# Performance work log

Measured on AMD Instinct MI355X. Metric: run time of the kernel, lower is better.

The kernel has to match this reference:

```python
import jax, jax.numpy as jnp
import numpy as np

# Config matching init_kwargs: input_shape=(C,T,H,W)=(512,32,14,14), window_size=9, n_heads=8
B, C, T, H, W = 2, 512, 32, 14, 14
N, K = 8, 9
CI = C // N              # per-head inter channels (64)
P = (K - 1) // 2         # symmetric temporal zero-pad so S == T


def setup_inputs() -> dict:
    key = jax.random.key(0)
    ks = jax.random.split(key, 7)
    s = 0.02
    return {
        "x":  jax.random.normal(ks[0], (B, C, T, H, W), jnp.float32),
        # per-head 1x1x1 conv (Linear3d) weights/biases, stacked over heads
        "Wq": jax.random.normal(ks[1], (N, CI, C), jnp.float32) * s,
        "bq": jax.random.normal(ks[2], (N, CI), jnp.float32) * s,
        "Wk": jax.random.normal(ks[3], (N, CI, C), jnp.float32) * s,
        "bk": jax.random.normal(ks[4], (N, CI), jnp.float32) * s,
        "Wv": jax.random.normal(ks[5], (N, CI, C), jnp.float32) * s,
        "bv": jax.random.normal(ks[6], (N, CI), jnp.float32) * s,
    }


def reference(x, Wq, bq, Wk, bk, Wv, bv):
    # x: (B, C, T, H, W). Dropout (p=0.25) is inference-mode identity.
    Bx, Cx, Tx, Hx, Wd = x.shape
    HW = Hx * Wd
    xf = x.reshape(Bx, Cx, Tx, HW)

    # Queries: every original frame is the center of its own window -> project x directly.
    q = jnp.einsum('bctp,nic->bnitp', xf, Wq) + bq[None, :, :, None, None]  # (B,N,ci,T,HW)

    # Keys/values on temporally zero-padded input (Pad3d gives S == T windows).
    xp = jnp.pad(xf, ((0, 0), (0, 0), (P, P), (0, 0)))  # (B,C,T+K-1,HW)
    k = jnp.einsum('bctp,nic->bnitp', xp, Wk) + bk[None, :, :, None, None]
    v = jnp.einsum('bctp,nic->bnitp', xp, Wv) + bv[None, :, :, None, None]

    # Sliding windows over padded time: window s covers padded frames s..s+K-1
    win = jnp.arange(Tx)[:, None] + jnp.arange(K)[None, :]  # (T,K)
    kw = k[:, :, :, win]  # (B,N,ci,T,K,HW)
    vw = v[:, :, :, win].reshape(Bx, N, CI, Tx, K * HW)

    # alpha[b,n,t,p,m] = sum_i q[b,n,i,t,p] * k_win[b,n,i,t,m]; softmax over keys m
    alpha = jnp.einsum('bnitp,bnitkm->bntpkm', q, kw).reshape(Bx, N, Tx, HW, K * HW)
    alpha = jax.nn.softmax(alpha, axis=-1)

    # y = alpha @ value -> (B,N,ci,T,HW); head concat is channel-major reshape
    y = jnp.einsum('bntpm,bnitm->bnitp', alpha, vw)
    z = y.reshape(Bx, Cx, Tx, Hx, Wd) + x  # residual
    return z
```

## Files before the change

kernel.cpp:

```cpp
#include <hip/hip_runtime.h>
#include <hip/hip_bf16.h>
#include <stdint.h>
#include <cstddef>

#define BB  2
#define CC  512
#define TT  32
#define HWP 196
#define NH  8
#define KWIN 9
#define CID 64
#define PPAD 4
#define TP  40
#define MTOT 12544
#define NTOT 1536
#define VSLOT 224
#define LOG2E 1.44269504f

typedef unsigned short u16;
typedef unsigned int   u32;
typedef __attribute__((ext_vector_type(8))) short short8;
typedef __attribute__((ext_vector_type(4))) float floatx4;

__device__ __forceinline__ u16 f2bf(float f) {
    u32 u = __float_as_uint(f);
    u32 r = (u + 0x7fffu + ((u >> 16) & 1u)) >> 16;
    return (u16)r;
}
__device__ __forceinline__ u32 pack2bf(float a, float b) {
    return (u32)f2bf(a) | ((u32)f2bf(b) << 16);
}
__device__ __forceinline__ u32 packtrunc(float a, float b) {
    return __builtin_amdgcn_perm(__float_as_uint(b), __float_as_uint(a), 0x07060302u);
}
__device__ __forceinline__ float fexp2(float x) {
    return __builtin_amdgcn_exp2f(x);
}
__device__ __forceinline__ void gload16(const u16* g, u16* l) {
    __builtin_amdgcn_global_load_lds(
        (const __attribute__((address_space(1))) u32*)g,
        (__attribute__((address_space(3))) u32*)l, 16, 0, 0);
}

__global__ __launch_bounds__(256) void prep_transpose(
    const float* __restrict__ x, u16* __restrict__ xt,
    const float* __restrict__ Wq, const float* __restrict__ Wk,
    const float* __restrict__ Wv, u16* __restrict__ Wbf,
    const float* __restrict__ bk, const float* __restrict__ bv,
    u16* __restrict__ Kout, u16* __restrict__ Vtp)
{
    __shared__ float T[64 * 197];
    int bxg = blockIdx.x;
    int tid = threadIdx.x;

    if (bxg < BB * TT * 8) {
        int bx = bxg;
        int ct = bx & 7; bx >>= 3;
        int t = bx & 31;
        int b = bx >> 5;
        const float* src = x + ((size_t)(b * CC + ct * 64) * TT + t) * HWP;
        for (int i = tid; i < 64 * 49; i += 256) {
            int c = i / 49;
            int p4 = i - c * 49;
            float4 v = *(const float4*)(src + (size_t)c * (TT * HWP) + p4 * 4);
            float* Tp = &T[c * 197 + p4 * 4];
            Tp[0] = v.x; Tp[1] = v.y; Tp[2] = v.z; Tp[3] = v.w;
        }
        __syncthreads();
        u16* dst = xt + (size_t)((b * TT + t) * HWP) * CC + ct * 64;
        for (int i = tid; i < HWP * 8; i += 256) {
            int p = i >> 3;
            int c0 = (i & 7) * 8;
            u32 w[4];
            #pragma unroll
            for (int k = 0; k < 4; k++)
                w[k] = pack2bf(T[(c0 + 2 * k) * 197 + p],
                               T[(c0 + 2 * k + 1) * 197 + p]);
            *(uint4*)(dst + (size_t)p * CC + c0) = *(uint4*)w;
        }
        return;
    }

    int id = (bxg - BB * TT * 8) * 256 + tid;
    const int wtot = NTOT * CC / 2;
    const int kper = 2 * NH * 8 * HWP * 32;
    const int vper = 2 * NH * 8 * 64 * (VSLOT/2);
    if (id < wtot) {
        int c2 = id & 255;
        int oc = id >> 8;
        int kind = oc >> 9;
        int idx = oc & 511;
        const float* src = (kind == 0 ? Wq : (kind == 1 ? Wk : Wv)) + (size_t)idx * CC + c2 * 2;
        ((u32*)Wbf)[id] = pack2bf(src[0], src[1]);
    } else if (id < wtot + kper) {
        int i = id - wtot;
        int ci2 = i & 31; i >>= 5;
        int p = i % HWP;  i /= HWP;
        int fr = i & 7;   i >>= 3;
        int head = i & 7;
        int b = i >> 3;
        int tp = fr < 4 ? fr : fr + 32;
        const float* bias = bk + head * CID + ci2 * 2;
        size_t addr = (((size_t)(b * NH + head) * TP + tp) * HWP + p) * 32 + ci2;
        ((u32*)Kout)[addr] = pack2bf(bias[0], bias[1]);
    } else if (id < wtot + kper + vper) {
        int i = id - wtot - kper;
        int s2 = i % (VSLOT/2); i /= (VSLOT/2);
        int ci = i & 63; i >>= 6;
        int fr = i & 7;  i >>= 3;
        int head = i & 7;
        int b = i >> 3;
        int tp = fr < 4 ? fr : fr + 32;
        float bias = bv[head * CID + ci];
        size_t addr = (((size_t)(b * NH + head) * TP + tp) * 64 + ci) * (VSLOT/2) + s2;
        ((u32*)Vtp)[addr] = pack2bf(bias, bias);
    }
}

__global__ __launch_bounds__(512) void proj_gemm2(
    const u16* __restrict__ xt, const u16* __restrict__ Wbf,
    const float* __restrict__ bq, const float* __restrict__ bk,
    const float* __restrict__ bv,
    u16* __restrict__ Qout, u16* __restrict__ Kout, u16* __restrict__ Vtp)
{
    __shared__ u16 sA[128 * 64];
    __shared__ u16 sB[256 * 64];

    int bx = blockIdx.x;
    int nb = bx % 6;
    int mt = bx / 6;
    int tid = threadIdx.x;
    int wave = tid >> 6, lane = tid & 63, quad = lane >> 4, l15 = lane & 15;
    int wm = wave >> 2, wn = wave & 3;
    int mbase = mt * 128 + wm * 64;
    int nbase = nb * 256 + wn * 64;

    int lr = lane >> 3;
    int sw = ((lane & 7) * 8) ^ (lr << 3);

    floatx4 acc[4][4];
    #pragma unroll
    for (int ms = 0; ms < 4; ms++)
        #pragma unroll
        for (int ns = 0; ns < 4; ns++)
            acc[ms][ns] = (floatx4){0.f, 0.f, 0.f, 0.f};

    const u16* abase = xt + (size_t)(mt * 128) * CC;
    const u16* bbase = Wbf + (size_t)(nb * 256) * CC;

    for (int kc = 0; kc < 8; kc++) {
        __syncthreads();
        #pragma unroll
        for (int i = 0; i < 2; i++) {
            int rbase = wave * 16 + i * 8;
            gload16(abase + (size_t)(rbase + lr) * CC + kc * 64 + sw,
                    &sA[rbase * 64]);
        }
        #pragma unroll
        for (int i = 0; i < 4; i++) {
            int rbase = wave * 32 + i * 8;
            gload16(bbase + (size_t)(rbase + lr) * CC + kc * 64 + sw,
                    &sB[rbase * 64]);
        }
        __syncthreads();

        #pragma unroll
        for (int kk = 0; kk < 2; kk++) {
            int swr = (kk * 32 + quad * 8) ^ ((l15 & 7) << 3);
            short8 af[4], bf[4];
            #pragma unroll
            for (int ms = 0; ms < 4; ms++)
                af[ms] = *(const short8*)&sA[(wm * 64 + ms * 16 + l15) * 64 + swr];
            #pragma unroll
            for (int ns = 0; ns < 4; ns++)
                bf[ns] = *(const short8*)&sB[(wn * 64 + ns * 16 + l15) * 64 + swr];
            #pragma unroll
            for (int ms = 0; ms < 4; ms++)
                #pragma unroll
                for (int ns = 0; ns < 4; ns++)
                    acc[ms][ns] = __builtin_amdgcn_mfma_f32_16x16x32_bf16(
                        af[ms], bf[ns], acc[ms][ns], 0, 0, 0);
        }
    }

    float biasv[4];
    #pragma unroll
    for (int ns = 0; ns < 4; ns++) {
        int n = nbase + ns * 16 + l15;
        int kind = n >> 9;
        int idx = n & 511;
        const float* bpb = kind == 0 ? bq : (kind == 1 ? bk : bv);
        biasv[ns] = bpb[idx];
    }

    #pragma unroll
    for (int ms = 0; ms < 4; ms++) {
        #pragma unroll
        for (int r = 0; r < 4; r++) {
            int m = mbase + ms * 16 + quad * 4 + r;
            int b = m / (TT * HWP);
            int rem = m - b * (TT * HWP);
            int t = rem / HWP;
            int p = rem - t * HWP;
            int slot_p = (p & ~31) | (p & 3) | (((p >> 4) & 1) << 2)
                       | (((p >> 2) & 1) << 3) | (((p >> 3) & 1) << 4);
            #pragma unroll
            for (int ns = 0; ns < 4; ns++) {
                int n = nbase + ns * 16 + l15;
                int kind = n >> 9;
                int idx = n & 511;
                int head = idx >> 6;
                int ci = idx & 63;
                float val = acc[ms][ns][r] + biasv[ns];
                if (kind == 0) {
                    Qout[(((size_t)(b * NH + head) * TT + t) * HWP + p) * CID + ci]
                        = f2bf(val * LOG2E);
                } else if (kind == 1) {
                    Kout[(((size_t)(b * NH + head) * TP + (t + PPAD)) * HWP + p) * CID + ci]
                        = f2bf(val);
                } else {
                    Vtp[(((size_t)(b * NH + head) * TP + (t + PPAD)) * 64 + ci) * VSLOT + slot_p]
                        = f2bf(val);
                }
            }
        }
    }
}

__global__ __launch_bounds__(256, 1) void attn_mfma4(
    const float* __restrict__ x,
    const u16* __restrict__ Qb, const u16* __restrict__ Kb,
    const u16* __restrict__ Vtp, float* __restrict__ zout)
{
    __shared__ float eT[HWP * 66];

    int i = blockIdx.x;
    int xcd = i & 7;
    int r = i >> 3;
    int slab = ((r >= 32) ? 8 : 0) | xcd;
    int t = r & 31;
    int b = slab >> 3, n = slab & 7;

    int tid = threadIdx.x;
    int wave = tid >> 6;
    int lane = tid & 63;
    int quad = lane >> 4, l15 = lane & 15;

    const u16* kfr0 = Kb + (size_t)slab * (TP * HWP) * CID;
    const u16* vslab = Vtp + (size_t)slab * (TP * 64 * VSLOT);
    const float tmask = (quad == 0) ? 1.0f : 0.0f;

    short8 qf[4][2];
    #pragma unroll
    for (int j = 0; j < 4; j++) {
        int qrow = (wave + 4 * j) * 16 + l15;
        qrow = qrow < HWP ? qrow : (HWP - 1);
        const u16* qp = Qb + ((size_t)(slab * TT + t) * HWP + qrow) * CID;
        qf[j][0] = *(const short8*)(qp + quad * 8);
        qf[j][1] = *(const short8*)(qp + 32 + quad * 8);
    }

    floatx4 acc[4][4];
    floatx4 accl[4];
    #pragma unroll
    for (int j = 0; j < 4; j++) {
        #pragma unroll
        for (int cg = 0; cg < 4; cg++) acc[j][cg] = (floatx4){0.f, 0.f, 0.f, 0.f};
        accl[j] = (floatx4){0.f, 0.f, 0.f, 0.f};
    }

    union { u32 w[4]; short8 s; } ones;
    ones.w[0] = 0x3F803F80u; ones.w[1] = 0x3F803F80u;
    ones.w[2] = 0x3F803F80u; ones.w[3] = 0x3F803F80u;

    #define KLOAD(c, D00, D01, D10, D11) do {                                    \
        const u16* a0_ = kfr0 + (size_t)(rbase + (c) * 32 + l15) * CID + quad * 8;\
        const u16* a1_ = a0_ + (size_t)16 * CID;                                 \
        D00 = *(const short8*)a0_;  D01 = *(const short8*)(a0_ + 32);            \
        D10 = *(const short8*)a1_;  D11 = *(const short8*)(a1_ + 32);            \
    } while (0)

    #define KLOADTAIL(D00, D01) do {                                             \
        int g_ = rbase + 192 + l15;                                              \
        g_ = g_ < (TP * HWP - 1) ? g_ : (TP * HWP - 1);                          \
        const u16* a0_ = kfr0 + (size_t)g_ * CID + quad * 8;                     \
        D00 = *(const short8*)a0_;  D01 = *(const short8*)(a0_ + 32);            \
    } while (0)

    #define VLOAD(c, D0, D1, D2, D3) do {                                        \
        const u16* v_ = vfr + l15 * VSLOT + (c) * 32 + quad * 8;                 \
        D0 = *(const short8*)v_;                                                 \
        D1 = *(const short8*)(v_ + 16 * VSLOT);                                  \
        D2 = *(const short8*)(v_ + 32 * VSLOT);                                  \
        D3 = *(const short8*)(v_ + 48 * VSLOT);                                  \
    } while (0)

    #define CHUNK_FULL(K00, K01, K10, K11, V0, V1, V2, V3)                       \
        _Pragma("unroll")                                                        \
        for (int j = 0; j < 4; j++) {                                            \
            floatx4 sc0 = (floatx4){0.f, 0.f, 0.f, 0.f};                         \
            sc0 = __builtin_amdgcn_mfma_f32_16x16x32_bf16(K00, qf[j][0], sc0, 0, 0, 0); \
            sc0 = __builtin_amdgcn_mfma_f32_16x16x32_bf16(K01, qf[j][1], sc0, 0, 0, 0); \
            floatx4 sc1 = (floatx4){0.f, 0.f, 0.f, 0.f};                         \
            sc1 = __builtin_amdgcn_mfma_f32_16x16x32_bf16(K10, qf[j][0], sc1, 0, 0, 0); \
            sc1 = __builtin_amdgcn_mfma_f32_16x16x32_bf16(K11, qf[j][1], sc1, 0, 0, 0); \
            union { u32 w[4]; short8 s; } pf;                                    \
            pf.w[0] = packtrunc(fexp2(sc0[0]), fexp2(sc0[1]));                   \
            pf.w[1] = packtrunc(fexp2(sc0[2]), fexp2(sc0[3]));                   \
            pf.w[2] = packtrunc(fexp2(sc1[0]), fexp2(sc1[1]));                   \
            pf.w[3] = packtrunc(fexp2(sc1[2]), fexp2(sc1[3]));                   \
            acc[j][0] = __builtin_amdgcn_mfma_f32_16x16x32_bf16(pf.s, V0, acc[j][0], 0, 0, 0); \
            acc[j][1] = __builtin_amdgcn_mfma_f32_16x16x32_bf16(pf.s, V1, acc[j][1], 0, 0, 0); \
            acc[j][2] = __builtin_amdgcn_mfma_f32_16x16x32_bf16(pf.s, V2, acc[j][2], 0, 0, 0); \
            acc[j][3] = __builtin_amdgcn_mfma_f32_16x16x32_bf16(pf.s, V3, acc[j][3], 0, 0, 0); \
            accl[j]   = __builtin_amdgcn_mfma_f32_16x16x32_bf16(pf.s, ones.s, accl[j], 0, 0, 0); \
        }

    #define CHUNK_TAIL(K00, K01, V0, V1, V2, V3)                                 \
        _Pragma("unroll")                                                        \
        for (int j = 0; j < 4; j++) {                                            \
            floatx4 sc0 = (floatx4){0.f, 0.f, 0.f, 0.f};                         \
            sc0 = __builtin_amdgcn_mfma_f32_16x16x32_bf16(K00, qf[j][0], sc0, 0, 0, 0); \
            sc0 = __builtin_amdgcn_mfma_f32_16x16x32_bf16(K01, qf[j][1], sc0, 0, 0, 0); \
            union { u32 w[4]; short8 s; } pf;                                    \
            pf.w[0] = packtrunc(fexp2(sc0[0]) * tmask, fexp2(sc0[1]) * tmask);   \
            pf.w[1] = packtrunc(fexp2(sc0[2]) * tmask, fexp2(sc0[3]) * tmask);   \
            pf.w[2] = 0u;                                                        \
            pf.w[3] = 0u;                                                        \
            acc[j][0] = __builtin_amdgcn_mfma_f32_16x16x32_bf16(pf.s, V0, acc[j][0], 0, 0, 0); \
            acc[j][1] = __builtin_amdgcn_mfma_f32_16x16x32_bf16(pf.s, V1, acc[j][1], 0, 0, 0); \
            acc[j][2] = __builtin_amdgcn_mfma_f32_16x16x32_bf16(pf.s, V2, acc[j][2], 0, 0, 0); \
            acc[j][3] = __builtin_amdgcn_mfma_f32_16x16x32_bf16(pf.s, V3, acc[j][3], 0, 0, 0); \
            accl[j]   = __builtin_amdgcn_mfma_f32_16x16x32_bf16(pf.s, ones.s, accl[j], 0, 0, 0); \
        }

    for (int f = 0; f < KWIN; f++) {
        int rbase = (t + f) * HWP;
        const u16* vfr = vslab + (size_t)(t + f) * (64 * VSLOT);

        short8 ka00, ka01, ka10, ka11, va0, va1, va2, va3;
        short8 kb00, kb01, kb10, kb11, vb0, vb1, vb2, vb3;
        short8 kc00, kc01, kc10, kc11, vc0, vc1, vc2, vc3;

        KLOAD(0, ka00, ka01, ka10, ka11);  VLOAD(0, va0, va1, va2, va3);
        KLOAD(1, kb00, kb01, kb10, kb11);  VLOAD(1, vb0, vb1, vb2, vb3);
        KLOAD(2, kc00, kc01, kc10, kc11);  VLOAD(2, vc0, vc1, vc2, vc3);
        CHUNK_FULL(ka00, ka01, ka10, ka11, va0, va1, va2, va3);
        KLOAD(3, ka00, ka01, ka10, ka11);  VLOAD(3, va0, va1, va2, va3);
        CHUNK_FULL(kb00, kb01, kb10, kb11, vb0, vb1, vb2, vb3);
        KLOAD(4, kb00, kb01, kb10, kb11);  VLOAD(4, vb0, vb1, vb2, vb3);
        CHUNK_FULL(kc00, kc01, kc10, kc11, vc0, vc1, vc2, vc3);
        KLOAD(5, kc00, kc01, kc10, kc11);  VLOAD(5, vc0, vc1, vc2, vc3);
        CHUNK_FULL(ka00, ka01, ka10, ka11, va0, va1, va2, va3);
        KLOADTAIL(ka00, ka01);             VLOAD(6, va0, va1, va2, va3);
        CHUNK_FULL(kb00, kb01, kb10, kb11, vb0, vb1, vb2, vb3);
        CHUNK_FULL(kc00, kc01, kc10, kc11, vc0, vc1, vc2, vc3);
        CHUNK_TAIL(ka00, ka01, va0, va1, va2, va3);
    }

    #undef KLOAD
    #undef KLOADTAIL
    #undef VLOAD
    #undef CHUNK_FULL
    #undef CHUNK_TAIL

    #pragma unroll
    for (int j = 0; j < 4; j++) {
        int tg = wave + 4 * j;
        float il[4];
        #pragma unroll
        for (int rr = 0; rr < 4; rr++) il[rr] = 1.0f / accl[j][rr];
        #pragma unroll
        for (int cg = 0; cg < 4; cg++) {
            #pragma unroll
            for (int rr = 0; rr < 4; rr++) {
                int p = tg * 16 + quad * 4 + rr;
                if (p < HWP)
                    eT[p * 66 + cg * 16 + l15] = acc[j][cg][rr] * il[rr];
            }
        }
    }
    __syncthreads();

    if (tid < HWP) {
        size_t base = ((size_t)(b * CC + n * CID) * TT + t) * HWP + tid;
        for (int ci = 0; ci < 64; ci++) {
            size_t a = base + (size_t)ci * (TT * HWP);
            zout[a] = eT[tid * 66 + ci] + x[a];
        }
    }
}

extern "C" void kernel_launch(void* const* d_in, const int* in_sizes, int n_in,
                              void* d_out, int out_size, void* d_ws, size_t ws_size,
                              hipStream_t stream) {
    const float* x  = (const float*)d_in[0];
    const float* Wq = (const float*)d_in[1];
    const float* bq = (const float*)d_in[2];
    const float* Wk = (const float*)d_in[3];
    const float* bk = (const float*)d_in[4];
    const float* Wv = (const float*)d_in[5];
    const float* bv = (const float*)d_in[6];
    float* z = (float*)d_out;

    const size_t qElems   = (size_t)BB * NH * TT * HWP * CID;
    const size_t kElems   = (size_t)BB * NH * TP * HWP * CID;
    const size_t vtpElems = (size_t)BB * NH * TP * 64 * VSLOT;

    u16* Qw  = (u16*)d_ws;
    u16* Kw  = Qw + qElems;
    u16* Vtp = Kw + kElems;
    u16* Wb  = Vtp + vtpElems;
    u16* Xt  = (u16*)d_out;

    {
        const int wtot = NTOT * CC / 2;
        const int kper = 2 * NH * 8 * HWP * 32;
        const int vper = 2 * NH * 8 * 64 * (VSLOT / 2);
        const int prepBlocks = (wtot + kper + vper + 255) / 256;
        prep_transpose<<<BB * TT * 8 + prepBlocks, 256, 0, stream>>>(
            x, Xt, Wq, Wk, Wv, Wb, bk, bv, Kw, Vtp);
    }
    proj_gemm2<<<98 * 6, 512, 0, stream>>>(Xt, Wb, bq, bk, bv, Qw, Kw, Vtp);
    attn_mfma4<<<512, 256, 0, stream>>>(x, Qw, Kw, Vtp, z);
}
```

Baseline: 242.0 us.

## Split the ragged 13th query tile across waves by key frame

Before, each of the 4 waves handled 4 query tiles of 16 rows, so the 13th tile (rows 192-207, only 4 valid) was computed redundantly by wave 0 at full cost. Now each wave keeps 3 full tiles, and the leftover tile is computed by one wave per key frame, chosen round-robin by frame index. The waves' partial numerators and denominators are then reduced through shared memory. This evens out work across the waves and drops the wasted tile compute, at the cost of extra shared-memory buffers and a small cross-wave reduction. It relies on softmax without max subtraction, so the partial sums can simply be added.

```diff
diff --git a/kernel.cpp b/kernel.cpp
--- a/kernel.cpp
+++ b/kernel.cpp
@@ -232,7 +232,9 @@
     const u16* __restrict__ Qb, const u16* __restrict__ Kb,
     const u16* __restrict__ Vtp, float* __restrict__ zout)
 {
-    __shared__ float eT[HWP * 66];
+    __shared__ float eT[192 * 66];
+    __shared__ float eT12[4][4][66];
+    __shared__ float ls12[4][4];
 
     int i = blockIdx.x;
     int xcd = i & 7;
@@ -250,24 +252,36 @@
     const u16* vslab = Vtp + (size_t)slab * (TP * 64 * VSLOT);
     const float tmask = (quad == 0) ? 1.0f : 0.0f;
 
-    short8 qf[4][2];
-    #pragma unroll
-    for (int j = 0; j < 4; j++) {
+    short8 qf[3][2];
+    #pragma unroll
+    for (int j = 0; j < 3; j++) {
         int qrow = (wave + 4 * j) * 16 + l15;
-        qrow = qrow < HWP ? qrow : (HWP - 1);
         const u16* qp = Qb + ((size_t)(slab * TT + t) * HWP + qrow) * CID;
         qf[j][0] = *(const short8*)(qp + quad * 8);
         qf[j][1] = *(const short8*)(qp + 32 + quad * 8);
     }
-
-    floatx4 acc[4][4];
-    floatx4 accl[4];
-    #pragma unroll
-    for (int j = 0; j < 4; j++) {
+    short8 qf12[2];
+    {
+        int qrow = 192 + l15;
+        qrow = qrow < HWP ? qrow : (HWP - 1);
+        const u16* qp = Qb + ((size_t)(slab * TT + t) * HWP + qrow) * CID;
+        qf12[0] = *(const short8*)(qp + quad * 8);
+        qf12[1] = *(const short8*)(qp + 32 + quad * 8);
+    }
+
+    floatx4 acc[3][4];
+    floatx4 accl[3];
+    floatx4 acc12[4];
+    floatx4 accl12;
+    #pragma unroll
+    for (int j = 0; j < 3; j++) {
         #pragma unroll
         for (int cg = 0; cg < 4; cg++) acc[j][cg] = (floatx4){0.f, 0.f, 0.f, 0.f};
         accl[j] = (floatx4){0.f, 0.f, 0.f, 0.f};
     }
+    #pragma unroll
+    for (int cg = 0; cg < 4; cg++) acc12[cg] = (floatx4){0.f, 0.f, 0.f, 0.f};
+    accl12 = (floatx4){0.f, 0.f, 0.f, 0.f};
 
     union { u32 w[4]; short8 s; } ones;
     ones.w[0] = 0x3F803F80u; ones.w[1] = 0x3F803F80u;
@@ -295,48 +309,65 @@
         D3 = *(const short8*)(v_ + 48 * VSLOT);                                  \
     } while (0)
 
-    #define CHUNK_FULL(K00, K01, K10, K11, V0, V1, V2, V3)                       \
+    #define CHUNK_ONE(Q0, Q1, ACC, ACCL, K00, K01, K10, K11, V0, V1, V2, V3) do {\
+        floatx4 sc0 = (floatx4){0.f, 0.f, 0.f, 0.f};                             \
+        sc0 = __builtin_amdgcn_mfma_f32_16x16x32_bf16(K00, Q0, sc0, 0, 0, 0);    \
+        sc0 = __builtin_amdgcn_mfma_f32_16x16x32_bf16(K01, Q1, sc0, 0, 0, 0);    \
+        floatx4 sc1 = (floatx4){0.f, 0.f, 0.f, 0.f};                             \
+        sc1 = __builtin_amdgcn_mfma_f32_16x16x32_bf16(K10, Q0, sc1, 0, 0, 0);    \
+        sc1 = __builtin_amdgcn_mfma_f32_16x16x32_bf16(K11, Q1, sc1, 0, 0, 0);    \
+        union { u32 w[4]; short8 s; } pf;                                        \
+        pf.w[0] = packtrunc(fexp2(sc0[0]), fexp2(sc0[1]));                       \
+        pf.w[1] = packtrunc(fexp2(sc0[2]), fexp2(sc0[3]));                       \
+        pf.w[2] = packtrunc(fexp2(sc1[0]), fexp2(sc1[1]));                       \
+        pf.w[3] = packtrunc(fexp2(sc1[2]), fexp2(sc1[3]));                       \
+        ACC[0] = __builtin_amdgcn_mfma_f32_16x16x32_bf16(pf.s, V0, ACC[0], 0, 0, 0); \
+        ACC[1] = __builtin_amdgcn_mfma_f32_16x16x32_bf16(pf.s, V1, ACC[1], 0, 0, 0); \
+        ACC[2] = __builtin_amdgcn_mfma_f32_16x16x32_bf16(pf.s, V2, ACC[2], 0, 0, 0); \
+        ACC[3] = __builtin_amdgcn_mfma_f32_16x16x32_bf16(pf.s, V3, ACC[3], 0, 0, 0); \
+        ACCL   = __builtin_amdgcn_mfma_f32_16x16x32_bf16(pf.s, ones.s, ACCL, 0, 0, 0); \
+    } while (0)
+
+    #define TAIL_ONE(Q0, Q1, ACC, ACCL, K00, K01, V0, V1, V2, V3) do {           \
+        floatx4 sc0 = (floatx4){0.f, 0.f, 0.f, 0.f};                             \
+        sc0 = __builtin_amdgcn_mfma_f32_16x16x32_bf16(K00, Q0, sc0, 0, 0, 0);    \
+        sc0 = __builtin_amdgcn_mfma_f32_16x16x32_bf16(K01, Q1, sc0, 0, 0, 0);    \
+        union { u32 w[4]; short8 s; } pf;                                        \
+        pf.w[0] = packtrunc(fexp2(sc0[0]) * tmask, fexp2(sc0[1]) * tmask);       \
+        pf.w[1] = packtrunc(fexp2(sc0[2]) * tmask, fexp2(sc0[3]) * tmask);       \
+        pf.w[2] = 0u;                                                            \
+        pf.w[3] = 0u;                                                            \
+        ACC[0] = __builtin_amdgcn_mfma_f32_16x16x32_bf16(pf.s, V0, ACC[0], 0, 0, 0); \
+        ACC[1] = __builtin_amdgcn_mfma_f32_16x16x32_bf16(pf.s, V1, ACC[1], 0, 0, 0); \
+        ACC[2] = __builtin_amdgcn_mfma_f32_16x16x32_bf16(pf.s, V2, ACC[2], 0, 0, 0); \
+        ACC[3] = __builtin_amdgcn_mfma_f32_16x16x32_bf16(pf.s, V3, ACC[3], 0, 0, 0); \
+        ACCL   = __builtin_amdgcn_mfma_f32_16x16x32_bf16(pf.s, ones.s, ACCL, 0, 0, 0); \
+    } while (0)
+
+    #define CHUNK_FULL(K00, K01, K10, K11, V0, V1, V2, V3) do {                  \
         _Pragma("unroll")                                                        \
-        for (int j = 0; j < 4; j++) {                                            \
-            floatx4 sc0 = (floatx4){0.f, 0.f, 0.f, 0.f};                         \
-            sc0 = __builtin_amdgcn_mfma_f32_16x16x32_bf16(K00, qf[j][0], sc0, 0, 0, 0); \
-            sc0 = __builtin_amdgcn_mfma_f32_16x16x32_bf16(K01, qf[j][1], sc0, 0, 0, 0); \
-            floatx4 sc1 = (floatx4){0.f, 0.f, 0.f, 0.f};                         \
-            sc1 = __builtin_amdgcn_mfma_f32_16x16x32_bf16(K10, qf[j][0], sc1, 0, 0, 0); \
-            sc1 = __builtin_amdgcn_mfma_f32_16x16x32_bf16(K11, qf[j][1], sc1, 0, 0, 0); \
-            union { u32 w[4]; short8 s; } pf;                                    \
-            pf.w[0] = packtrunc(fexp2(sc0[0]), fexp2(sc0[1]));                   \
-            pf.w[1] = packtrunc(fexp2(sc0[2]), fexp2(sc0[3]));                   \
-            pf.w[2] = packtrunc(fexp2(sc1[0]), fexp2(sc1[1]));                   \
-            pf.w[3] = packtrunc(fexp2(sc1[2]), fexp2(sc1[3]));                   \
-            acc[j][0] = __builtin_amdgcn_mfma_f32_16x16x32_bf16(pf.s, V0, acc[j][0], 0, 0, 0); \
-            acc[j][1] = __builtin_amdgcn_mfma_f32_16x16x32_bf16(pf.s, V1, acc[j][1], 0, 0, 0); \
-            acc[j][2] = __builtin_amdgcn_mfma_f32_16x16x32_bf16(pf.s, V2, acc[j][2], 0, 0, 0); \
-            acc[j][3] = __builtin_amdgcn_mfma_f32_16x16x32_bf16(pf.s, V3, acc[j][3], 0, 0, 0); \
-            accl[j]   = __builtin_amdgcn_mfma_f32_16x16x32_bf16(pf.s, ones.s, accl[j], 0, 0, 0); \
-        }
-
-    #define CHUNK_TAIL(K00, K01, V0, V1, V2, V3)                                 \
+        for (int j = 0; j < 3; j++)                                              \
+            CHUNK_ONE(qf[j][0], qf[j][1], acc[j], accl[j],                       \
+                      K00, K01, K10, K11, V0, V1, V2, V3);                       \
+        if (do12)                                                                \
+            CHUNK_ONE(qf12[0], qf12[1], acc12, accl12,                           \
+                      K00, K01, K10, K11, V0, V1, V2, V3);                       \
+    } while (0)
+
+    #define CHUNK_TAIL(K00, K01, V0, V1, V2, V3) do {                            \
         _Pragma("unroll")                                                        \
-        for (int j = 0; j < 4; j++) {                                            \
-            floatx4 sc0 = (floatx4){0.f, 0.f, 0.f, 0.f};                         \
-            sc0 = __builtin_amdgcn_mfma_f32_16x16x32_bf16(K00, qf[j][0], sc0, 0, 0, 0); \
-            sc0 = __builtin_amdgcn_mfma_f32_16x16x32_bf16(K01, qf[j][1], sc0, 0, 0, 0); \
-            union { u32 w[4]; short8 s; } pf;                                    \
-            pf.w[0] = packtrunc(fexp2(sc0[0]) * tmask, fexp2(sc0[1]) * tmask);   \
-            pf.w[1] = packtrunc(fexp2(sc0[2]) * tmask, fexp2(sc0[3]) * tmask);   \
-            pf.w[2] = 0u;                                                        \
-            pf.w[3] = 0u;                                                        \
-            acc[j][0] = __builtin_amdgcn_mfma_f32_16x16x32_bf16(pf.s, V0, acc[j][0], 0, 0, 0); \
-            acc[j][1] = __builtin_amdgcn_mfma_f32_16x16x32_bf16(pf.s, V1, acc[j][1], 0, 0, 0); \
-            acc[j][2] = __builtin_amdgcn_mfma_f32_16x16x32_bf16(pf.s, V2, acc[j][2], 0, 0, 0); \
-            acc[j][3] = __builtin_amdgcn_mfma_f32_16x16x32_bf16(pf.s, V3, acc[j][3], 0, 0, 0); \
-            accl[j]   = __builtin_amdgcn_mfma_f32_16x16x32_bf16(pf.s, ones.s, accl[j], 0, 0, 0); \
-        }
+        for (int j = 0; j < 3; j++)                                              \
+            TAIL_ONE(qf[j][0], qf[j][1], acc[j], accl[j],                        \
+                     K00, K01, V0, V1, V2, V3);                                  \
+        if (do12)                                                                \
+            TAIL_ONE(qf12[0], qf12[1], acc12, accl12,                            \
+                     K00, K01, V0, V1, V2, V3);                                  \
+    } while (0)
 
     for (int f = 0; f < KWIN; f++) {
         int rbase = (t + f) * HWP;
         const u16* vfr = vslab + (size_t)(t + f) * (64 * VSLOT);
+        bool do12 = ((f & 3) == wave);
 
         short8 ka00, ka01, ka10, ka11, va0, va1, va2, va3;
         short8 kb00, kb01, kb10, kb11, vb0, vb1, vb2, vb3;
@@ -361,11 +392,13 @@
     #undef KLOAD
     #undef KLOADTAIL
     #undef VLOAD
+    #undef CHUNK_ONE
+    #undef TAIL_ONE
     #undef CHUNK_FULL
     #undef CHUNK_TAIL
 
     #pragma unroll
-    for (int j = 0; j < 4; j++) {
+    for (int j = 0; j < 3; j++) {
         int tg = wave + 4 * j;
         float il[4];
         #pragma unroll
@@ -375,18 +408,38 @@
             #pragma unroll
             for (int rr = 0; rr < 4; rr++) {
                 int p = tg * 16 + quad * 4 + rr;
-                if (p < HWP)
-                    eT[p * 66 + cg * 16 + l15] = acc[j][cg][rr] * il[rr];
+                eT[p * 66 + cg * 16 + l15] = acc[j][cg][rr] * il[rr];
             }
+        }
+    }
+    if (quad == 0) {
+        #pragma unroll
+        for (int rr = 0; rr < 4; rr++) {
+            #pragma unroll
+            for (int cg = 0; cg < 4; cg++)
+                eT12[wave][rr][cg * 16 + l15] = acc12[cg][rr];
+            if (l15 == 0) ls12[wave][rr] = accl12[rr];
         }
     }
     __syncthreads();
 
     if (tid < HWP) {
         size_t base = ((size_t)(b * CC + n * CID) * TT + t) * HWP + tid;
-        for (int ci = 0; ci < 64; ci++) {
-            size_t a = base + (size_t)ci * (TT * HWP);
-            zout[a] = eT[tid * 66 + ci] + x[a];
+        if (tid < 192) {
+            for (int ci = 0; ci < 64; ci++) {
+                size_t a = base + (size_t)ci * (TT * HWP);
+                zout[a] = eT[tid * 66 + ci] + x[a];
+            }
+        } else {
+            int rr = tid - 192;
+            float l = ls12[0][rr] + ls12[1][rr] + ls12[2][rr] + ls12[3][rr];
+            float il = 1.0f / l;
+            for (int ci = 0; ci < 64; ci++) {
+                size_t a = base + (size_t)ci * (TT * HWP);
+                float v = (eT12[0][rr][ci] + eT12[1][rr][ci]
+                         + eT12[2][rr][ci] + eT12[3][rr][ci]) * il;
+                zout[a] = v + x[a];
+            }
         }
     }
 }
```

New measurement: 239.3 us (median of 2 runs). No clear change (-1.1%).
